# Kernel optimization log

Measured on AMD Instinct MI355X. Metric: run time of the kernel, lower is better.

Reference implementation:

```python
import jax, jax.numpy as jnp
import numpy as np
import math

B, NPG, DEG = 100, 500, 12          # graphs, nodes/graph, avg degree
F_IN, H, C = 128, 128, 10
RATIO = 0.5
N = B * NPG
E = N * DEG
K1 = math.ceil(NPG * RATIO)          # 250
K2 = math.ceil(K1 * RATIO)           # 125
K3 = math.ceil(K2 * RATIO)           # 63


def _lin(k, i, o):
    return jax.random.uniform(k, (i, o), jnp.float32, -1.0, 1.0) / np.sqrt(i).astype(np.float32)


def setup_inputs() -> dict:
    key = jax.random.key(0)
    ks = jax.random.split(key, 16)
    x = jax.random.normal(ks[0], (N, F_IN), jnp.float32)
    off = (jnp.arange(B, dtype=jnp.int32) * NPG)[:, None]
    src = (jax.random.randint(ks[1], (B, NPG * DEG), 0, NPG, jnp.int32) + off).reshape(-1)
    dst = (jax.random.randint(ks[2], (B, NPG * DEG), 0, NPG, jnp.int32) + off).reshape(-1)
    edge_index = jnp.stack([src, dst])
    return {
        'x': x, 'edge_index': edge_index,
        'Wl1': _lin(ks[3], F_IN, H), 'bl1': jnp.zeros((H,), jnp.float32), 'Wr1': _lin(ks[4], F_IN, H),
        'Wl2': _lin(ks[5], H, H), 'bl2': jnp.zeros((H,), jnp.float32), 'Wr2': _lin(ks[6], H, H),
        'Wl3': _lin(ks[7], H, H), 'bl3': jnp.zeros((H,), jnp.float32), 'Wr3': _lin(ks[8], H, H),
        'pw1': jax.random.normal(ks[9], (H,), jnp.float32),
        'pw2': jax.random.normal(ks[10], (H,), jnp.float32),
        'pw3': jax.random.normal(ks[11], (H,), jnp.float32),
        'W1': _lin(ks[12], 2 * H, H), 'b1': jnp.zeros((H,), jnp.float32),
        'W2': _lin(ks[13], H, H // 2), 'b2': jnp.zeros((H // 2,), jnp.float32),
        'W3': _lin(ks[14], H // 2, C), 'b3': jnp.zeros((C,), jnp.float32),
    }


def sage_conv(x, src, dst, emask, Wl, bl, Wr, n_nodes):
    # PyG SAGEConv: out_i = lin_l(mean_{j->i} x_j) + lin_r(x_i)
    msg = x[src] * emask[:, None]                                   # [E, d]
    agg = jax.ops.segment_sum(msg, dst, num_segments=n_nodes)
    cnt = jax.ops.segment_sum(emask, dst, num_segments=n_nodes)
    mean = agg / jnp.maximum(cnt, 1.0)[:, None]
    return mean @ Wl + bl + x @ Wr


def topk_pool(x, w, src, dst, emask, n_per, k):
    # TopKPooling: score = tanh(x.w/||w||); keep top-k nodes per graph; x_kept *= score
    score = jnp.tanh((x @ w) / jnp.linalg.norm(w))                  # [B*n_per]
    topv, topi = jax.lax.top_k(score.reshape(B, n_per), k)          # [B, k]
    perm = (topi + (jnp.arange(B, dtype=jnp.int32) * n_per)[:, None]).reshape(-1)
    x_new = x[perm] * topv.reshape(-1)[:, None]                     # [B*k, d]
    mapping = jnp.full((B * n_per,), -1, jnp.int32).at[perm].set(jnp.arange(B * k, dtype=jnp.int32))
    ns, nd = mapping[src], mapping[dst]
    emask_new = emask * ((ns >= 0) & (nd >= 0)).astype(emask.dtype)
    return x_new, jnp.maximum(ns, 0), jnp.maximum(nd, 0), emask_new


def readout(x, k):
    # global_max_pool || global_mean_pool (all graphs have exactly k nodes)
    xr = x.reshape(B, k, H)
    return jnp.concatenate([xr.max(axis=1), xr.mean(axis=1)], axis=1)  # [B, 2H]


def reference(x, edge_index, Wl1, bl1, Wr1, Wl2, bl2, Wr2, Wl3, bl3, Wr3,
              pw1, pw2, pw3, W1, b1, W2, b2, W3, b3):
    src, dst = edge_index[0], edge_index[1]
    emask = jnp.ones((E,), jnp.float32)
    h = jax.nn.relu(sage_conv(x, src, dst, emask, Wl1, bl1, Wr1, N))
    h, src, dst, emask = topk_pool(h, pw1, src, dst, emask, NPG, K1)
    x1 = readout(h, K1)
    h = jax.nn.relu(sage_conv(h, src, dst, emask, Wl2, bl2, Wr2, B * K1))
    h, src, dst, emask = topk_pool(h, pw2, src, dst, emask, K1, K2)
    x2 = readout(h, K2)
    h = jax.nn.relu(sage_conv(h, src, dst, emask, Wl3, bl3, Wr3, B * K2))
    h, src, dst, emask = topk_pool(h, pw3, src, dst, emask, K2, K3)
    x3 = readout(h, K3)
    z = x1 + x2 + x3
    z = jax.nn.relu(z @ W1 + b1)   # dropout is identity in eval mode
    z = jax.nn.relu(z @ W2 + b2)
    return jax.nn.log_softmax(z @ W3 + b3, axis=1)   # pool_loss == 0 for TopKPool
```

## Files before the change

kernel.cpp:

```cpp
#include <hip/hip_runtime.h>
#include <math.h>

#define BG    100
#define NPG   500
#define FD    128
#define EE    600000
#define EPG   6000
#define NN    50000
#define K1    250
#define K2    125
#define K3    63
#define CAP   64

typedef short v8s __attribute__((ext_vector_type(8)));
typedef float v4f __attribute__((ext_vector_type(4)));

__device__ __forceinline__ int swz(int p, int N) {
    int j = p & 7, i = p >> 3;
    int chunk = N >> 3, rem = N & 7;
    int mj = j < rem ? j : rem;
    return j * chunk + mj + i;
}

__device__ __forceinline__ unsigned short f2bf(float f) {
    unsigned int u = __float_as_uint(f);
    unsigned int r = (u + 0x7FFFu + ((u >> 16) & 1u)) >> 16;
    return (unsigned short)r;
}
__device__ __forceinline__ float bf2f(unsigned short b) {
    return __uint_as_float(((unsigned int)b) << 16);
}

__global__ __launch_bounds__(1024) void prep_fill_kernel(
        const int* __restrict__ ei, int* __restrict__ deg, int* __restrict__ col,
        const float* __restrict__ Wl1, const float* __restrict__ Wr1,
        const float* __restrict__ Wl2, const float* __restrict__ Wr2,
        const float* __restrict__ Wl3, const float* __restrict__ Wr3,
        unsigned short* __restrict__ wt_hi, unsigned short* __restrict__ wt_lo) {
    __shared__ int lcnt[NPG];
    int tid = threadIdx.x;
    if (blockIdx.x < BG) {
        int b = swz(blockIdx.x, BG);
        for (int i = tid; i < NPG; i += 1024) lcnt[i] = 0;
        __syncthreads();
        for (int e0 = tid; e0 < EPG; e0 += 1024) {
            int e = b * EPG + e0;
            int d = ei[EE + e];
            int pos = atomicAdd(&lcnt[d - b * NPG], 1);
            if (pos < CAP) col[(long long)d * CAP + pos] = ei[e];
        }
        __syncthreads();
        for (int i = tid; i < NPG; i += 1024) deg[b * NPG + i] = lcnt[i];
    } else {
        int id = (blockIdx.x - BG) * 1024 + tid;
        if (id >= 3 * 256 * 128) return;
        int layer = id >> 15, rem = id & 32767;
        int k = rem >> 7, n = rem & 127;
        const float* Wl = layer == 0 ? Wl1 : (layer == 1 ? Wl2 : Wl3);
        const float* Wr = layer == 0 ? Wr1 : (layer == 1 ? Wr2 : Wr3);
        float w = (k < 128) ? Wl[k * 128 + n] : Wr[(k - 128) * 128 + n];
        unsigned short hi = f2bf(w);
        unsigned short lo = f2bf(w - bf2f(hi));
        long long o = (long long)layer * 32768
                    + (long long)(k >> 5) * 4096
                    + (long long)(n >> 4) * 512
                    + (long long)((k >> 3) & 3) * 128
                    + (long long)(n & 15) * 8
                    + (k & 7);
        wt_hi[o] = hi;
        wt_lo[o] = lo;
    }
}

__global__ void gather_agg_kernel(const int* __restrict__ deg, const int* __restrict__ col,
                                  const float* __restrict__ x, float* __restrict__ mean,
                                  int n, int NB) {
    int g = swz(blockIdx.x, NB) * 256 + threadIdx.x;
    int node = g >> 5, sub = g & 31;
    if (node >= n) return;
    int d = deg[node]; if (d > CAP) d = CAP;
    const int* cp = col + (long long)node * CAP;
    float ax = 0.0f, ay = 0.0f, az = 0.0f, aw = 0.0f;
    int j = 0;
    for (; j + 8 <= d; j += 8) {
        float4 v0 = ((const float4*)(x + (long long)cp[j]     * FD))[sub];
        float4 v1 = ((const float4*)(x + (long long)cp[j + 1] * FD))[sub];
        float4 v2 = ((const float4*)(x + (long long)cp[j + 2] * FD))[sub];
        float4 v3 = ((const float4*)(x + (long long)cp[j + 3] * FD))[sub];
        float4 v4 = ((const float4*)(x + (long long)cp[j + 4] * FD))[sub];
        float4 v5 = ((const float4*)(x + (long long)cp[j + 5] * FD))[sub];
        float4 v6 = ((const float4*)(x + (long long)cp[j + 6] * FD))[sub];
        float4 v7 = ((const float4*)(x + (long long)cp[j + 7] * FD))[sub];
        ax += v0.x; ay += v0.y; az += v0.z; aw += v0.w;
        ax += v1.x; ay += v1.y; az += v1.z; aw += v1.w;
        ax += v2.x; ay += v2.y; az += v2.z; aw += v2.w;
        ax += v3.x; ay += v3.y; az += v3.z; aw += v3.w;
        ax += v4.x; ay += v4.y; az += v4.z; aw += v4.w;
        ax += v5.x; ay += v5.y; az += v5.z; aw += v5.w;
        ax += v6.x; ay += v6.y; az += v6.z; aw += v6.w;
        ax += v7.x; ay += v7.y; az += v7.z; aw += v7.w;
    }
    for (; j + 4 <= d; j += 4) {
        float4 v0 = ((const float4*)(x + (long long)cp[j]     * FD))[sub];
        float4 v1 = ((const float4*)(x + (long long)cp[j + 1] * FD))[sub];
        float4 v2 = ((const float4*)(x + (long long)cp[j + 2] * FD))[sub];
        float4 v3 = ((const float4*)(x + (long long)cp[j + 3] * FD))[sub];
        ax += v0.x; ay += v0.y; az += v0.z; aw += v0.w;
        ax += v1.x; ay += v1.y; az += v1.z; aw += v1.w;
        ax += v2.x; ay += v2.y; az += v2.z; aw += v2.w;
        ax += v3.x; ay += v3.y; az += v3.z; aw += v3.w;
    }
    for (; j < d; ++j) {
        float4 v = ((const float4*)(x + (long long)cp[j] * FD))[sub];
        ax += v.x; ay += v.y; az += v.z; aw += v.w;
    }
    float inv = 1.0f / fmaxf((float)d, 1.0f);
    float4 o; o.x = ax * inv; o.y = ay * inv; o.z = az * inv; o.w = aw * inv;
    ((float4*)(mean + (long long)node * FD))[sub] = o;
}

__global__ __launch_bounds__(512) void sage_gemm_mfma_kernel(
        const float* __restrict__ mean, const float* __restrict__ x,
        const unsigned short* __restrict__ wt_hi, const unsigned short* __restrict__ wt_lo,
        const float* __restrict__ bl, const float* __restrict__ pw,
        float* __restrict__ hout, float* __restrict__ score, int M, int NB) {
    __shared__ unsigned short Bh[4096], Bl[4096];
    __shared__ float spart[128 * 16];
    __shared__ float snrmp[16];
    int tid  = threadIdx.x;
    int wave = tid >> 6, lane = tid & 63;
    int quad = lane >> 4, l15 = lane & 15;
    int row0 = swz(blockIdx.x, NB) * 128;

    v4f acc[8];
#pragma unroll
    for (int t = 0; t < 8; t++) acc[t] = (v4f){0.f, 0.f, 0.f, 0.f};

    if (tid < 16) {
        float s = 0.f;
#pragma unroll
        for (int t = 0; t < 8; t++) { float p = pw[t * 16 + tid]; s += p * p; }
        snrmp[tid] = s;
    }

    int growA = row0 + 16 * wave + l15; if (growA > M - 1) growA = M - 1;

    for (int kt = 0; kt < 8; ++kt) {
        uint4 gh = ((const uint4*)(wt_hi + kt * 4096))[tid];
        uint4 gl = ((const uint4*)(wt_lo + kt * 4096))[tid];
        const float* Ab = (kt < 4) ? mean : x;
        const float* ap = Ab + (long long)growA * FD + ((kt < 4) ? kt : kt - 4) * 32 + quad * 8;
        float4 v0 = *(const float4*)(ap);
        float4 v1 = *(const float4*)(ap + 4);
        *(uint4*)&Bh[tid * 8] = gh;
        *(uint4*)&Bl[tid * 8] = gl;
        float f[8] = {v0.x, v0.y, v0.z, v0.w, v1.x, v1.y, v1.z, v1.w};
        v8s a_h, a_l;
#pragma unroll
        for (int q = 0; q < 8; q++) {
            unsigned short hb = f2bf(f[q]);
            a_h[q] = (short)hb;
            a_l[q] = (short)f2bf(f[q] - bf2f(hb));
        }
        __syncthreads();
#pragma unroll
        for (int t = 0; t < 8; t++) {
            v8s b_h = *(const v8s*)&Bh[t * 512 + lane * 8];
            v8s b_l = *(const v8s*)&Bl[t * 512 + lane * 8];
            acc[t] = __builtin_amdgcn_mfma_f32_16x16x32_bf16(a_l, b_h, acc[t], 0, 0, 0);
            acc[t] = __builtin_amdgcn_mfma_f32_16x16x32_bf16(a_h, b_l, acc[t], 0, 0, 0);
            acc[t] = __builtin_amdgcn_mfma_f32_16x16x32_bf16(a_h, b_h, acc[t], 0, 0, 0);
        }
        __syncthreads();
    }

    int rbase = row0 + 16 * wave + quad * 4;
    float part[4] = {0.f, 0.f, 0.f, 0.f};
#pragma unroll
    for (int t = 0; t < 8; t++) {
        int colc = t * 16 + l15;
        float blv = bl[colc];
        float pwv = pw[colc];
#pragma unroll
        for (int reg = 0; reg < 4; reg++) {
            float h = fmaxf(acc[t][reg] + blv, 0.0f);
            part[reg] += h * pwv;
            int grow = rbase + reg;
            if (grow < M) hout[(long long)grow * FD + colc] = h;
        }
    }
#pragma unroll
    for (int reg = 0; reg < 4; reg++)
        spart[(16 * wave + quad * 4 + reg) * 16 + l15] = part[reg];
    __syncthreads();
    if (tid < 128) {
        int grow = row0 + tid;
        if (grow < M) {
            float dot = 0.0f;
#pragma unroll
            for (int i = 0; i < 16; i++) dot += spart[tid * 16 + i];
            float nr = 0.0f;
#pragma unroll
            for (int i = 0; i < 16; i++) nr += snrmp[i];
            score[grow] = tanhf(dot / sqrtf(nr));
        }
    }
}

__global__ __launch_bounds__(1024) void topk_tail_kernel(
        const float* __restrict__ score, const float* __restrict__ hout,
        int n_per, int k, int SN,
        float* __restrict__ xp,
        const int* __restrict__ esrc, const int* __restrict__ edst,
        int* __restrict__ gmap,
        int* __restrict__ next_deg, int* __restrict__ next_col,
        float* __restrict__ z, int mode,
        const float* __restrict__ W1, const float* __restrict__ b1,
        const float* __restrict__ W2, const float* __restrict__ b2,
        const float* __restrict__ W3, const float* __restrict__ b3,
        float* __restrict__ out) {
    __shared__ float skey[512];
    __shared__ int   sidx[512];
    __shared__ unsigned long long spk[512];
    __shared__ int   lmap[512];
    __shared__ int   lcnt[512];
    __shared__ float pmax[1024];
    __shared__ float psum[1024];
    __shared__ float zs[256], t1[128], t2[64], t3[16];
    int tid = threadIdx.x;
    int kind, b;
    if (mode == 2) { kind = 1; b = swz(blockIdx.x, BG); }
    else {
        kind = blockIdx.x >= BG ? 1 : 0;
        b = swz(kind ? blockIdx.x - BG : blockIdx.x, BG);
    }

    if (kind == 0)
        for (int i = tid; i < SN; i += 1024) { lmap[i] = -1; lcnt[i] = 0; }

    unsigned long long P = 0ULL;
    if (tid < SN) {
        float keyv; unsigned int idx;
        if (tid < n_per) { keyv = score[b * n_per + tid]; idx = (unsigned int)tid; }
        else             { keyv = -INFINITY;              idx = 0x7fffffffu; }
        unsigned int u = __float_as_uint(keyv);
        u = (u & 0x80000000u) ? ~u : (u | 0x80000000u);
        P = ((unsigned long long)u << 32) | (unsigned long long)(~idx);
    }
    for (int ks = 2; ks <= SN; ks <<= 1) {
        for (int j = ks >> 1; j > 0; j >>= 1) {
            unsigned long long Q;
            if (j >= 64) {
                __syncthreads();
                if (tid < SN) spk[tid] = P;
                __syncthreads();
                Q = (tid < SN) ? spk[tid ^ j] : 0ULL;
            } else {
                Q = __shfl_xor(P, j, 64);
            }
            if (tid < SN) {
                bool keepmax = (((tid & ks) == 0) == ((tid & j) == 0));
                if (keepmax == (Q > P)) P = Q;
            }
        }
    }
    if (tid < SN) {
        unsigned int u  = (unsigned int)(P >> 32);
        unsigned int fb = (u & 0x80000000u) ? (u & 0x7fffffffu) : ~u;
        int iv = (int)(~(unsigned int)P);
        skey[tid] = __uint_as_float(fb);
        sidx[tid] = iv;
        if (kind == 0 && tid < k) lmap[iv] = tid;
    }
    __syncthreads();

    if (kind == 0) {
        int kbase = b * k;
        if (mode == 0) {
            int nbase = b * n_per;
            for (int e0 = tid; e0 < EPG; e0 += 1024) {
                int e = b * EPG + e0;
                int ls = lmap[esrc[e] - nbase];
                int ld = lmap[edst[e] - nbase];
                if (ls >= 0 && ld >= 0) {
                    int pos = atomicAdd(&lcnt[ld], 1);
                    if (pos < CAP) next_col[(long long)(kbase + ld) * CAP + pos] = kbase + ls;
                }
            }
            __syncthreads();
            for (int i = tid; i < NPG; i += 1024) {
                int l = lmap[i];
                gmap[nbase + i] = l >= 0 ? kbase + l : -1;
            }
        } else {
            int kb1 = b * n_per;
            for (int e0 = tid; e0 < EPG; e0 += 1024) {
                int e = b * EPG + e0;
                int ws = gmap[esrc[e]];
                int wd = gmap[edst[e]];
                int ls = (ws >= 0) ? lmap[ws - kb1] : -1;
                int ld = (wd >= 0) ? lmap[wd - kb1] : -1;
                if (ls >= 0 && ld >= 0) {
                    int pos = atomicAdd(&lcnt[ld], 1);
                    if (pos < CAP) next_col[(long long)(kbase + ld) * CAP + pos] = kbase + ls;
                }
            }
            __syncthreads();
        }
        for (int i = tid; i < k; i += 1024) next_deg[kbase + i] = lcnt[i];
        return;
    }

    int c = tid & 127, s = tid >> 7;
    float mx = -INFINITY, sm = 0.0f;
    {
        int r = s;
        long long hbase = (long long)b * n_per * FD + c;
        long long xbase = (long long)b * k * FD + c;
        for (; r + 24 < k; r += 32) {
            int i0 = sidx[r], i1 = sidx[r + 8], i2 = sidx[r + 16], i3 = sidx[r + 24];
            float k0 = skey[r], k1 = skey[r + 8], k2 = skey[r + 16], k3 = skey[r + 24];
            float v0 = hout[hbase + (long long)i0 * FD] * k0;
            float v1 = hout[hbase + (long long)i1 * FD] * k1;
            float v2 = hout[hbase + (long long)i2 * FD] * k2;
            float v3 = hout[hbase + (long long)i3 * FD] * k3;
            if (mode != 2) {
                xp[xbase + (long long)(r)      * FD] = v0;
                xp[xbase + (long long)(r + 8)  * FD] = v1;
                xp[xbase + (long long)(r + 16) * FD] = v2;
                xp[xbase + (long long)(r + 24) * FD] = v3;
            }
            mx = fmaxf(mx, v0); sm += v0;
            mx = fmaxf(mx, v1); sm += v1;
            mx = fmaxf(mx, v2); sm += v2;
            mx = fmaxf(mx, v3); sm += v3;
        }
        for (; r < k; r += 8) {
            float v = hout[hbase + (long long)sidx[r] * FD] * skey[r];
            if (mode != 2) xp[xbase + (long long)r * FD] = v;
            mx = fmaxf(mx, v); sm += v;
        }
    }
    pmax[tid] = mx; psum[tid] = sm;
    __syncthreads();
    if (tid < 128) {
        float m = -INFINITY, su = 0.0f;
#pragma unroll
        for (int i = 0; i < 8; i++) {
            m = fmaxf(m, pmax[i * 128 + tid]);
            su += psum[i * 128 + tid];
        }
        float mean = su / (float)k;
        if (mode == 0)      { z[b * 256 + tid] = m;  z[b * 256 + 128 + tid] = mean;  }
        else if (mode == 1) { z[b * 256 + tid] += m; z[b * 256 + 128 + tid] += mean; }
        else {
            zs[tid]       = z[b * 256 + tid] + m;
            zs[128 + tid] = z[b * 256 + 128 + tid] + mean;
        }
    }
    if (mode == 2) {
        __syncthreads();
        if (tid < 128) {
            float a = b1[tid];
            for (int kk = 0; kk < 256; kk++) a += zs[kk] * W1[kk * 128 + tid];
            t1[tid] = fmaxf(a, 0.0f);
        }
        __syncthreads();
        if (tid < 64) {
            float a = b2[tid];
            for (int kk = 0; kk < 128; kk++) a += t1[kk] * W2[kk * 64 + tid];
            t2[tid] = fmaxf(a, 0.0f);
        }
        __syncthreads();
        if (tid < 10) {
            float a = b3[tid];
            for (int kk = 0; kk < 64; kk++) a += t2[kk] * W3[kk * 10 + tid];
            t3[tid] = a;
        }
        __syncthreads();
        if (tid == 0) {
            float m = -INFINITY;
            for (int i = 0; i < 10; i++) m = fmaxf(m, t3[i]);
            float su = 0.0f;
            for (int i = 0; i < 10; i++) su += expf(t3[i] - m);
            float ls = logf(su);
            for (int i = 0; i < 10; i++) out[b * 10 + i] = t3[i] - m - ls;
        }
    }
}

extern "C" void kernel_launch(void* const* d_in, const int* in_sizes, int n_in,
                              void* d_out, int out_size, void* d_ws, size_t ws_size,
                              hipStream_t stream) {
    (void)in_sizes; (void)n_in; (void)out_size; (void)ws_size;
    const float* x   = (const float*)d_in[0];
    const int*   ei  = (const int*)d_in[1];
    const float* Wl1 = (const float*)d_in[2];
    const float* bl1 = (const float*)d_in[3];
    const float* Wr1 = (const float*)d_in[4];
    const float* Wl2 = (const float*)d_in[5];
    const float* bl2 = (const float*)d_in[6];
    const float* Wr2 = (const float*)d_in[7];
    const float* Wl3 = (const float*)d_in[8];
    const float* bl3 = (const float*)d_in[9];
    const float* Wr3 = (const float*)d_in[10];
    const float* pw1 = (const float*)d_in[11];
    const float* pw2 = (const float*)d_in[12];
    const float* pw3 = (const float*)d_in[13];
    const float* W1  = (const float*)d_in[14];
    const float* b1  = (const float*)d_in[15];
    const float* W2  = (const float*)d_in[16];
    const float* b2  = (const float*)d_in[17];
    const float* W3  = (const float*)d_in[18];
    const float* b3  = (const float*)d_in[19];
    float* out = (float*)d_out;

    char* ws = (char*)d_ws;
    size_t off = 0;
    auto alloc = [&](size_t bytes) {
        char* p = ws + off;
        off = (off + bytes + 255) & ~(size_t)255;
        return p;
    };
    float* mean  = (float*)alloc((size_t)NN * FD * 4);
    float* hout  = (float*)alloc((size_t)NN * FD * 4);
    float* xp    = (float*)alloc((size_t)BG * K1 * FD * 4);
    float* sc    = (float*)alloc((size_t)NN * 4);
    int*   gmap  = (int*)  alloc((size_t)NN * 4);
    int*   deg   = (int*)  alloc((size_t)NN * 4);
    int*   colb  = (int*)  alloc((size_t)NN * CAP * 4);
    float* z     = (float*)alloc((size_t)BG * 256 * 4);
    unsigned short* wt_hi = (unsigned short*)alloc((size_t)3 * 32768 * 2);
    unsigned short* wt_lo = (unsigned short*)alloc((size_t)3 * 32768 * 2);

    prep_fill_kernel<<<BG + 96, 1024, 0, stream>>>(ei, deg, colb,
                                                   Wl1, Wr1, Wl2, Wr2, Wl3, Wr3, wt_hi, wt_lo);

    {
        int nb = (NN * 32 + 255) / 256;
        gather_agg_kernel<<<nb, 256, 0, stream>>>(deg, colb, x, mean, NN, nb);
    }
    {
        int nb = (NN + 127) / 128;
        sage_gemm_mfma_kernel<<<nb, 512, 0, stream>>>(mean, x, wt_hi, wt_lo,
                                                      bl1, pw1, hout, sc, NN, nb);
    }
    topk_tail_kernel<<<2 * BG, 1024, 0, stream>>>(sc, hout, NPG, K1, 512, xp,
                                                  ei, ei + EE, gmap, deg, colb,
                                                  z, 0, W1, b1, W2, b2, W3, b3, out);

    const int N2 = BG * K1;
    {
        int nb = (N2 * 32 + 255) / 256;
        gather_agg_kernel<<<nb, 256, 0, stream>>>(deg, colb, xp, mean, N2, nb);
    }
    {
        int nb = (N2 + 127) / 128;
        sage_gemm_mfma_kernel<<<nb, 512, 0, stream>>>(mean, xp, wt_hi + 32768, wt_lo + 32768,
                                                      bl2, pw2, hout, sc, N2, nb);
    }
    topk_tail_kernel<<<2 * BG, 1024, 0, stream>>>(sc, hout, K1, K2, 256, xp,
                                                  ei, ei + EE, gmap, deg, colb,
                                                  z, 1, W1, b1, W2, b2, W3, b3, out);

    const int N3 = BG * K2;
    {
        int nb = (N3 * 32 + 255) / 256;
        gather_agg_kernel<<<nb, 256, 0, stream>>>(deg, colb, xp, mean, N3, nb);
    }
    {
        int nb = (N3 + 127) / 128;
        sage_gemm_mfma_kernel<<<nb, 512, 0, stream>>>(mean, xp, wt_hi + 65536, wt_lo + 65536,
                                                      bl3, pw3, hout, sc, N3, nb);
    }
    topk_tail_kernel<<<BG, 1024, 0, stream>>>(sc, hout, K2, K3, 128, (float*)0,
                                              (const int*)0, (const int*)0, (int*)0,
                                              (int*)0, (int*)0,
                                              z, 2, W1, b1, W2, b2, W3, b3, out);
}
```

Measured before the change: 250.7 us.

## Fuse neighbor mean aggregation into SAGE MFMA GEMM kernel

Removes the separate gather/aggregate kernel and computes each 128-row tile's neighbor mean inside the GEMM kernel. Rows are staged 16 at a time through a shared slab, and each wave keeps its mean fragment in registers for the first four K-tiles. This avoids writing and re-reading the full mean buffer in global memory and saves a launch per layer. In exchange, the gather now runs with fewer concurrent waves, has 16 block-wide barriers per tile, and adds 32 floats of register pressure per thread, which may reduce latency hiding on the random gathers.

After: 270.8 us. 1.08x slower.

```diff
diff --git a/kernel.cpp b/kernel.cpp
--- a/kernel.cpp
+++ b/kernel.cpp
@@ -72,59 +72,14 @@
     }
 }
 
-__global__ void gather_agg_kernel(const int* __restrict__ deg, const int* __restrict__ col,
-                                  const float* __restrict__ x, float* __restrict__ mean,
-                                  int n, int NB) {
-    int g = swz(blockIdx.x, NB) * 256 + threadIdx.x;
-    int node = g >> 5, sub = g & 31;
-    if (node >= n) return;
-    int d = deg[node]; if (d > CAP) d = CAP;
-    const int* cp = col + (long long)node * CAP;
-    float ax = 0.0f, ay = 0.0f, az = 0.0f, aw = 0.0f;
-    int j = 0;
-    for (; j + 8 <= d; j += 8) {
-        float4 v0 = ((const float4*)(x + (long long)cp[j]     * FD))[sub];
-        float4 v1 = ((const float4*)(x + (long long)cp[j + 1] * FD))[sub];
-        float4 v2 = ((const float4*)(x + (long long)cp[j + 2] * FD))[sub];
-        float4 v3 = ((const float4*)(x + (long long)cp[j + 3] * FD))[sub];
-        float4 v4 = ((const float4*)(x + (long long)cp[j + 4] * FD))[sub];
-        float4 v5 = ((const float4*)(x + (long long)cp[j + 5] * FD))[sub];
-        float4 v6 = ((const float4*)(x + (long long)cp[j + 6] * FD))[sub];
-        float4 v7 = ((const float4*)(x + (long long)cp[j + 7] * FD))[sub];
-        ax += v0.x; ay += v0.y; az += v0.z; aw += v0.w;
-        ax += v1.x; ay += v1.y; az += v1.z; aw += v1.w;
-        ax += v2.x; ay += v2.y; az += v2.z; aw += v2.w;
-        ax += v3.x; ay += v3.y; az += v3.z; aw += v3.w;
-        ax += v4.x; ay += v4.y; az += v4.z; aw += v4.w;
-        ax += v5.x; ay += v5.y; az += v5.z; aw += v5.w;
-        ax += v6.x; ay += v6.y; az += v6.z; aw += v6.w;
-        ax += v7.x; ay += v7.y; az += v7.z; aw += v7.w;
-    }
-    for (; j + 4 <= d; j += 4) {
-        float4 v0 = ((const float4*)(x + (long long)cp[j]     * FD))[sub];
-        float4 v1 = ((const float4*)(x + (long long)cp[j + 1] * FD))[sub];
-        float4 v2 = ((const float4*)(x + (long long)cp[j + 2] * FD))[sub];
-        float4 v3 = ((const float4*)(x + (long long)cp[j + 3] * FD))[sub];
-        ax += v0.x; ay += v0.y; az += v0.z; aw += v0.w;
-        ax += v1.x; ay += v1.y; az += v1.z; aw += v1.w;
-        ax += v2.x; ay += v2.y; az += v2.z; aw += v2.w;
-        ax += v3.x; ay += v3.y; az += v3.z; aw += v3.w;
-    }
-    for (; j < d; ++j) {
-        float4 v = ((const float4*)(x + (long long)cp[j] * FD))[sub];
-        ax += v.x; ay += v.y; az += v.z; aw += v.w;
-    }
-    float inv = 1.0f / fmaxf((float)d, 1.0f);
-    float4 o; o.x = ax * inv; o.y = ay * inv; o.z = az * inv; o.w = aw * inv;
-    ((float4*)(mean + (long long)node * FD))[sub] = o;
-}
-
-__global__ __launch_bounds__(512) void sage_gemm_mfma_kernel(
-        const float* __restrict__ mean, const float* __restrict__ x,
+__global__ __launch_bounds__(512) void sage_gemm_fused_kernel(
+        const int* __restrict__ deg, const int* __restrict__ col,
+        const float* __restrict__ x,
         const unsigned short* __restrict__ wt_hi, const unsigned short* __restrict__ wt_lo,
         const float* __restrict__ bl, const float* __restrict__ pw,
         float* __restrict__ hout, float* __restrict__ score, int M, int NB) {
     __shared__ unsigned short Bh[4096], Bl[4096];
+    __shared__ float mslab[16 * 132];
     __shared__ float spart[128 * 16];
     __shared__ float snrmp[16];
     int tid  = threadIdx.x;
@@ -145,11 +100,93 @@
 
     int growA = row0 + 16 * wave + l15; if (growA > M - 1) growA = M - 1;
 
-    for (int kt = 0; kt < 8; ++kt) {
+    float macc[32];
+    {
+        int rlocal = tid >> 5;
+        int sub    = tid & 31;
+        for (int rg = 0; rg < 8; ++rg) {
+            int row = row0 + rg * 16 + rlocal;
+            int d = (row < M) ? deg[row] : 0;
+            if (d > CAP) d = CAP;
+            const int* cp = col + (long long)row * CAP;
+            float ax = 0.0f, ay = 0.0f, az = 0.0f, aw = 0.0f;
+            int j = 0;
+            for (; j + 8 <= d; j += 8) {
+                float4 v0 = ((const float4*)(x + (long long)cp[j]     * FD))[sub];
+                float4 v1 = ((const float4*)(x + (long long)cp[j + 1] * FD))[sub];
+                float4 v2 = ((const float4*)(x + (long long)cp[j + 2] * FD))[sub];
+                float4 v3 = ((const float4*)(x + (long long)cp[j + 3] * FD))[sub];
+                float4 v4 = ((const float4*)(x + (long long)cp[j + 4] * FD))[sub];
+                float4 v5 = ((const float4*)(x + (long long)cp[j + 5] * FD))[sub];
+                float4 v6 = ((const float4*)(x + (long long)cp[j + 6] * FD))[sub];
+                float4 v7 = ((const float4*)(x + (long long)cp[j + 7] * FD))[sub];
+                ax += v0.x; ay += v0.y; az += v0.z; aw += v0.w;
+                ax += v1.x; ay += v1.y; az += v1.z; aw += v1.w;
+                ax += v2.x; ay += v2.y; az += v2.z; aw += v2.w;
+                ax += v3.x; ay += v3.y; az += v3.z; aw += v3.w;
+                ax += v4.x; ay += v4.y; az += v4.z; aw += v4.w;
+                ax += v5.x; ay += v5.y; az += v5.z; aw += v5.w;
+                ax += v6.x; ay += v6.y; az += v6.z; aw += v6.w;
+                ax += v7.x; ay += v7.y; az += v7.z; aw += v7.w;
+            }
+            for (; j + 4 <= d; j += 4) {
+                float4 v0 = ((const float4*)(x + (long long)cp[j]     * FD))[sub];
+                float4 v1 = ((const float4*)(x + (long long)cp[j + 1] * FD))[sub];
+                float4 v2 = ((const float4*)(x + (long long)cp[j + 2] * FD))[sub];
+                float4 v3 = ((const float4*)(x + (long long)cp[j + 3] * FD))[sub];
+                ax += v0.x; ay += v0.y; az += v0.z; aw += v0.w;
+                ax += v1.x; ay += v1.y; az += v1.z; aw += v1.w;
+                ax += v2.x; ay += v2.y; az += v2.z; aw += v2.w;
+                ax += v3.x; ay += v3.y; az += v3.z; aw += v3.w;
+            }
+            for (; j < d; ++j) {
+                float4 v = ((const float4*)(x + (long long)cp[j] * FD))[sub];
+                ax += v.x; ay += v.y; az += v.z; aw += v.w;
+            }
+            float inv = 1.0f / fmaxf((float)d, 1.0f);
+            float4 o; o.x = ax * inv; o.y = ay * inv; o.z = az * inv; o.w = aw * inv;
+            *(float4*)&mslab[rlocal * 132 + sub * 4] = o;
+            __syncthreads();
+            if (wave == rg) {
+#pragma unroll
+                for (int kt = 0; kt < 4; ++kt)
+#pragma unroll
+                    for (int q = 0; q < 8; ++q)
+                        macc[kt * 8 + q] = mslab[l15 * 132 + quad * 8 + kt * 32 + q];
+            }
+            __syncthreads();
+        }
+    }
+
+#pragma unroll
+    for (int kt = 0; kt < 4; ++kt) {
         uint4 gh = ((const uint4*)(wt_hi + kt * 4096))[tid];
         uint4 gl = ((const uint4*)(wt_lo + kt * 4096))[tid];
-        const float* Ab = (kt < 4) ? mean : x;
-        const float* ap = Ab + (long long)growA * FD + ((kt < 4) ? kt : kt - 4) * 32 + quad * 8;
+        *(uint4*)&Bh[tid * 8] = gh;
+        *(uint4*)&Bl[tid * 8] = gl;
+        v8s a_h, a_l;
+#pragma unroll
+        for (int q = 0; q < 8; q++) {
+            float fv = macc[kt * 8 + q];
+            unsigned short hb = f2bf(fv);
+            a_h[q] = (short)hb;
+            a_l[q] = (short)f2bf(fv - bf2f(hb));
+        }
+        __syncthreads();
+#pragma unroll
+        for (int t = 0; t < 8; t++) {
+            v8s b_h = *(const v8s*)&Bh[t * 512 + lane * 8];
+            v8s b_l = *(const v8s*)&Bl[t * 512 + lane * 8];
+            acc[t] = __builtin_amdgcn_mfma_f32_16x16x32_bf16(a_l, b_h, acc[t], 0, 0, 0);
+            acc[t] = __builtin_amdgcn_mfma_f32_16x16x32_bf16(a_h, b_l, acc[t], 0, 0, 0);
+            acc[t] = __builtin_amdgcn_mfma_f32_16x16x32_bf16(a_h, b_h, acc[t], 0, 0, 0);
+        }
+        __syncthreads();
+    }
+    for (int kt = 4; kt < 8; ++kt) {
+        uint4 gh = ((const uint4*)(wt_hi + kt * 4096))[tid];
+        uint4 gl = ((const uint4*)(wt_lo + kt * 4096))[tid];
+        const float* ap = x + (long long)growA * FD + (kt - 4) * 32 + quad * 8;
         float4 v0 = *(const float4*)(ap);
         float4 v1 = *(const float4*)(ap + 4);
         *(uint4*)&Bh[tid * 8] = gh;
@@ -422,7 +459,6 @@
         off = (off + bytes + 255) & ~(size_t)255;
         return p;
     };
-    float* mean  = (float*)alloc((size_t)NN * FD * 4);
     float* hout  = (float*)alloc((size_t)NN * FD * 4);
     float* xp    = (float*)alloc((size_t)BG * K1 * FD * 4);
     float* sc    = (float*)alloc((size_t)NN * 4);
@@ -437,13 +473,9 @@
                                                    Wl1, Wr1, Wl2, Wr2, Wl3, Wr3, wt_hi, wt_lo);
 
     {
-        int nb = (NN * 32 + 255) / 256;
-        gather_agg_kernel<<<nb, 256, 0, stream>>>(deg, colb, x, mean, NN, nb);
-    }
-    {
         int nb = (NN + 127) / 128;
-        sage_gemm_mfma_kernel<<<nb, 512, 0, stream>>>(mean, x, wt_hi, wt_lo,
-                                                      bl1, pw1, hout, sc, NN, nb);
+        sage_gemm_fused_kernel<<<nb, 512, 0, stream>>>(deg, colb, x, wt_hi, wt_lo,
+                                                       bl1, pw1, hout, sc, NN, nb);
     }
     topk_tail_kernel<<<2 * BG, 1024, 0, stream>>>(sc, hout, NPG, K1, 512, xp,
                                                   ei, ei + EE, gmap, deg, colb,
@@ -451,13 +483,9 @@
 
     const int N2 = BG * K1;
     {
-        int nb = (N2 * 32 + 255) / 256;
-        gather_agg_kernel<<<nb, 256, 0, stream>>>(deg, colb, xp, mean, N2, nb);
-    }
-    {
         int nb = (N2 + 127) / 128;
-        sage_gemm_mfma_kernel<<<nb, 512, 0, stream>>>(mean, xp, wt_hi + 32768, wt_lo + 32768,
-                                                      bl2, pw2, hout, sc, N2, nb);
+        sage_gemm_fused_kernel<<<nb, 512, 0, stream>>>(deg, colb, xp, wt_hi + 32768, wt_lo + 32768,
+                                                       bl2, pw2, hout, sc, N2, nb);
     }
     topk_tail_kernel<<<2 * BG, 1024, 0, stream>>>(sc, hout, K1, K2, 256, xp,
                                                   ei, ei + EE, gmap, deg, colb,
@@ -465,13 +493,9 @@
 
     const int N3 = BG * K2;
     {
-        int nb = (N3 * 32 + 255) / 256;
-        gather_agg_kernel<<<nb, 256, 0, stream>>>(deg, colb, xp, mean, N3, nb);
-    }
-    {
         int nb = (N3 + 127) / 128;
-        sage_gemm_mfma_kernel<<<nb, 512, 0, stream>>>(mean, xp, wt_hi + 65536, wt_lo + 65536,
-                                                      bl3, pw3, hout, sc, N3, nb);
+        sage_gemm_fused_kernel<<<nb, 512, 0, stream>>>(deg, colb, xp, wt_hi + 65536, wt_lo + 65536,
+                                                       bl3, pw3, hout, sc, N3, nb);
     }
     topk_tail_kernel<<<BG, 1024, 0, stream>>>(sc, hout, K2, K3, 128, (float*)0,
                                               (const int*)0, (const int*)0, (int*)0,
```

## Fuse pooling, layers 2-3 and MLP head into one per-graph kernel

Applied to the files above, without the earlier changes.

Replaces the three top-k tail kernels and the layer-2 and layer-3 gather and GEMM launches with a single kernel of one 1024-thread block per graph. Each block runs sort, edge remap, pooling, neighbour aggregation, the MFMA GEMM and the final MLP in sequence. The node remap stays in shared memory, and the next layer's scores stay on-chip instead of going through global memory. This removes several launches and global round trips. In exchange, the later layers run on only 100 blocks, so the gather and GEMM work gets less parallelism across the GPU.

After: 253.3 us. About the same (+1.0%).

```diff
diff --git a/kernel.cpp b/kernel.cpp
--- a/kernel.cpp
+++ b/kernel.cpp
@@ -207,42 +207,14 @@
     }
 }
 
-__global__ __launch_bounds__(1024) void topk_tail_kernel(
-        const float* __restrict__ score, const float* __restrict__ hout,
-        int n_per, int k, int SN,
-        float* __restrict__ xp,
-        const int* __restrict__ esrc, const int* __restrict__ edst,
-        int* __restrict__ gmap,
-        int* __restrict__ next_deg, int* __restrict__ next_col,
-        float* __restrict__ z, int mode,
-        const float* __restrict__ W1, const float* __restrict__ b1,
-        const float* __restrict__ W2, const float* __restrict__ b2,
-        const float* __restrict__ W3, const float* __restrict__ b3,
-        float* __restrict__ out) {
-    __shared__ float skey[512];
-    __shared__ int   sidx[512];
-    __shared__ unsigned long long spk[512];
-    __shared__ int   lmap[512];
-    __shared__ int   lcnt[512];
-    __shared__ float pmax[1024];
-    __shared__ float psum[1024];
-    __shared__ float zs[256], t1[128], t2[64], t3[16];
-    int tid = threadIdx.x;
-    int kind, b;
-    if (mode == 2) { kind = 1; b = swz(blockIdx.x, BG); }
-    else {
-        kind = blockIdx.x >= BG ? 1 : 0;
-        b = swz(kind ? blockIdx.x - BG : blockIdx.x, BG);
-    }
-
-    if (kind == 0)
-        for (int i = tid; i < SN; i += 1024) { lmap[i] = -1; lcnt[i] = 0; }
-
+
+__device__ __forceinline__ void sort_phase(const float* scoreSrc, int n_per, int SN, int tid,
+        unsigned long long* spk, float* skey, int* sidx, int* lmap, int kset) {
     unsigned long long P = 0ULL;
     if (tid < SN) {
         float keyv; unsigned int idx;
-        if (tid < n_per) { keyv = score[b * n_per + tid]; idx = (unsigned int)tid; }
-        else             { keyv = -INFINITY;              idx = 0x7fffffffu; }
+        if (tid < n_per) { keyv = scoreSrc[tid]; idx = (unsigned int)tid; }
+        else             { keyv = -INFINITY;     idx = 0x7fffffffu; }
         unsigned int u = __float_as_uint(keyv);
         u = (u & 0x80000000u) ? ~u : (u | 0x80000000u);
         P = ((unsigned long long)u << 32) | (unsigned long long)(~idx);
@@ -270,76 +242,38 @@
         int iv = (int)(~(unsigned int)P);
         skey[tid] = __uint_as_float(fb);
         sidx[tid] = iv;
-        if (kind == 0 && tid < k) lmap[iv] = tid;
-    }
-    __syncthreads();
-
-    if (kind == 0) {
-        int kbase = b * k;
-        if (mode == 0) {
-            int nbase = b * n_per;
-            for (int e0 = tid; e0 < EPG; e0 += 1024) {
-                int e = b * EPG + e0;
-                int ls = lmap[esrc[e] - nbase];
-                int ld = lmap[edst[e] - nbase];
-                if (ls >= 0 && ld >= 0) {
-                    int pos = atomicAdd(&lcnt[ld], 1);
-                    if (pos < CAP) next_col[(long long)(kbase + ld) * CAP + pos] = kbase + ls;
-                }
-            }
-            __syncthreads();
-            for (int i = tid; i < NPG; i += 1024) {
-                int l = lmap[i];
-                gmap[nbase + i] = l >= 0 ? kbase + l : -1;
-            }
-        } else {
-            int kb1 = b * n_per;
-            for (int e0 = tid; e0 < EPG; e0 += 1024) {
-                int e = b * EPG + e0;
-                int ws = gmap[esrc[e]];
-                int wd = gmap[edst[e]];
-                int ls = (ws >= 0) ? lmap[ws - kb1] : -1;
-                int ld = (wd >= 0) ? lmap[wd - kb1] : -1;
-                if (ls >= 0 && ld >= 0) {
-                    int pos = atomicAdd(&lcnt[ld], 1);
-                    if (pos < CAP) next_col[(long long)(kbase + ld) * CAP + pos] = kbase + ls;
-                }
-            }
-            __syncthreads();
-        }
-        for (int i = tid; i < k; i += 1024) next_deg[kbase + i] = lcnt[i];
-        return;
-    }
-
+        if (tid < kset) lmap[iv] = tid;
+    }
+}
+
+__device__ __forceinline__ void pool_phase(const float* __restrict__ hb, float* __restrict__ xb,
+        const float* skey, const int* sidx, float* pmax, float* psum,
+        float* zsum, float* zs, int k, int tid, int mode) {
     int c = tid & 127, s = tid >> 7;
     float mx = -INFINITY, sm = 0.0f;
-    {
-        int r = s;
-        long long hbase = (long long)b * n_per * FD + c;
-        long long xbase = (long long)b * k * FD + c;
-        for (; r + 24 < k; r += 32) {
-            int i0 = sidx[r], i1 = sidx[r + 8], i2 = sidx[r + 16], i3 = sidx[r + 24];
-            float k0 = skey[r], k1 = skey[r + 8], k2 = skey[r + 16], k3 = skey[r + 24];
-            float v0 = hout[hbase + (long long)i0 * FD] * k0;
-            float v1 = hout[hbase + (long long)i1 * FD] * k1;
-            float v2 = hout[hbase + (long long)i2 * FD] * k2;
-            float v3 = hout[hbase + (long long)i3 * FD] * k3;
-            if (mode != 2) {
-                xp[xbase + (long long)(r)      * FD] = v0;
-                xp[xbase + (long long)(r + 8)  * FD] = v1;
-                xp[xbase + (long long)(r + 16) * FD] = v2;
-                xp[xbase + (long long)(r + 24) * FD] = v3;
-            }
-            mx = fmaxf(mx, v0); sm += v0;
-            mx = fmaxf(mx, v1); sm += v1;
-            mx = fmaxf(mx, v2); sm += v2;
-            mx = fmaxf(mx, v3); sm += v3;
-        }
-        for (; r < k; r += 8) {
-            float v = hout[hbase + (long long)sidx[r] * FD] * skey[r];
-            if (mode != 2) xp[xbase + (long long)r * FD] = v;
-            mx = fmaxf(mx, v); sm += v;
-        }
+    int r = s;
+    for (; r + 24 < k; r += 32) {
+        int i0 = sidx[r], i1 = sidx[r + 8], i2 = sidx[r + 16], i3 = sidx[r + 24];
+        float k0 = skey[r], k1 = skey[r + 8], k2 = skey[r + 16], k3 = skey[r + 24];
+        float v0 = hb[c + (long long)i0 * FD] * k0;
+        float v1 = hb[c + (long long)i1 * FD] * k1;
+        float v2 = hb[c + (long long)i2 * FD] * k2;
+        float v3 = hb[c + (long long)i3 * FD] * k3;
+        if (xb) {
+            xb[c + (long long)(r)      * FD] = v0;
+            xb[c + (long long)(r + 8)  * FD] = v1;
+            xb[c + (long long)(r + 16) * FD] = v2;
+            xb[c + (long long)(r + 24) * FD] = v3;
+        }
+        mx = fmaxf(mx, v0); sm += v0;
+        mx = fmaxf(mx, v1); sm += v1;
+        mx = fmaxf(mx, v2); sm += v2;
+        mx = fmaxf(mx, v3); sm += v3;
+    }
+    for (; r < k; r += 8) {
+        float v = hb[c + (long long)sidx[r] * FD] * skey[r];
+        if (xb) xb[c + (long long)r * FD] = v;
+        mx = fmaxf(mx, v); sm += v;
     }
     pmax[tid] = mx; psum[tid] = sm;
     __syncthreads();
@@ -351,41 +285,276 @@
             su += psum[i * 128 + tid];
         }
         float mean = su / (float)k;
-        if (mode == 0)      { z[b * 256 + tid] = m;  z[b * 256 + 128 + tid] = mean;  }
-        else if (mode == 1) { z[b * 256 + tid] += m; z[b * 256 + 128 + tid] += mean; }
-        else {
-            zs[tid]       = z[b * 256 + tid] + m;
-            zs[128 + tid] = z[b * 256 + 128 + tid] + mean;
-        }
-    }
-    if (mode == 2) {
+        if (mode == 0)      { zsum[tid] = m;  zsum[128 + tid] = mean;  }
+        else if (mode == 1) { zsum[tid] += m; zsum[128 + tid] += mean; }
+        else { zs[tid] = zsum[tid] + m; zs[128 + tid] = zsum[128 + tid] + mean; }
+    }
+}
+
+__device__ __forceinline__ void gather_phase(const int* lcnt, const int* __restrict__ colX,
+        const float* __restrict__ xsrc, float* __restrict__ meanX,
+        int kbase, int k, int tid) {
+    int sub = tid & 31;
+    for (int base = 0; base < k; base += 32) {
+        int nl = base + (tid >> 5);
+        if (nl < k) {
+            int d = lcnt[nl]; if (d > CAP) d = CAP;
+            const int* cp = colX + (long long)(kbase + nl) * CAP;
+            float ax = 0.0f, ay = 0.0f, az = 0.0f, aw = 0.0f;
+            int j = 0;
+            for (; j + 8 <= d; j += 8) {
+                float4 v0 = ((const float4*)(xsrc + (long long)cp[j]     * FD))[sub];
+                float4 v1 = ((const float4*)(xsrc + (long long)cp[j + 1] * FD))[sub];
+                float4 v2 = ((const float4*)(xsrc + (long long)cp[j + 2] * FD))[sub];
+                float4 v3 = ((const float4*)(xsrc + (long long)cp[j + 3] * FD))[sub];
+                float4 v4 = ((const float4*)(xsrc + (long long)cp[j + 4] * FD))[sub];
+                float4 v5 = ((const float4*)(xsrc + (long long)cp[j + 5] * FD))[sub];
+                float4 v6 = ((const float4*)(xsrc + (long long)cp[j + 6] * FD))[sub];
+                float4 v7 = ((const float4*)(xsrc + (long long)cp[j + 7] * FD))[sub];
+                ax += v0.x; ay += v0.y; az += v0.z; aw += v0.w;
+                ax += v1.x; ay += v1.y; az += v1.z; aw += v1.w;
+                ax += v2.x; ay += v2.y; az += v2.z; aw += v2.w;
+                ax += v3.x; ay += v3.y; az += v3.z; aw += v3.w;
+                ax += v4.x; ay += v4.y; az += v4.z; aw += v4.w;
+                ax += v5.x; ay += v5.y; az += v5.z; aw += v5.w;
+                ax += v6.x; ay += v6.y; az += v6.z; aw += v6.w;
+                ax += v7.x; ay += v7.y; az += v7.z; aw += v7.w;
+            }
+            for (; j + 4 <= d; j += 4) {
+                float4 v0 = ((const float4*)(xsrc + (long long)cp[j]     * FD))[sub];
+                float4 v1 = ((const float4*)(xsrc + (long long)cp[j + 1] * FD))[sub];
+                float4 v2 = ((const float4*)(xsrc + (long long)cp[j + 2] * FD))[sub];
+                float4 v3 = ((const float4*)(xsrc + (long long)cp[j + 3] * FD))[sub];
+                ax += v0.x; ay += v0.y; az += v0.z; aw += v0.w;
+                ax += v1.x; ay += v1.y; az += v1.z; aw += v1.w;
+                ax += v2.x; ay += v2.y; az += v2.z; aw += v2.w;
+                ax += v3.x; ay += v3.y; az += v3.z; aw += v3.w;
+            }
+            for (; j < d; ++j) {
+                float4 v = ((const float4*)(xsrc + (long long)cp[j] * FD))[sub];
+                ax += v.x; ay += v.y; az += v.z; aw += v.w;
+            }
+            float inv = 1.0f / fmaxf((float)d, 1.0f);
+            float4 o; o.x = ax * inv; o.y = ay * inv; o.z = az * inv; o.w = aw * inv;
+            ((float4*)(meanX + (long long)(kbase + nl) * FD))[sub] = o;
+        }
+    }
+}
+
+__device__ __forceinline__ void gemm_phase(const float* __restrict__ meanX,
+        const float* __restrict__ xsrc,
+        const unsigned short* __restrict__ wh, const unsigned short* __restrict__ wl,
+        const float* __restrict__ blv, const float* __restrict__ pwv,
+        float* __restrict__ hX, float* scoreL, float* snrmp,
+        unsigned short* Bh, unsigned short* Bl, float* spart,
+        int kbase, int krows, int tid, int wave, int lane, int quad, int l15) {
+    v4f acc[8];
+#pragma unroll
+    for (int t = 0; t < 8; t++) acc[t] = (v4f){0.f, 0.f, 0.f, 0.f};
+    if (tid < 16) {
+        float s = 0.f;
+#pragma unroll
+        for (int t = 0; t < 8; t++) { float p = pwv[t * 16 + tid]; s += p * p; }
+        snrmp[tid] = s;
+    }
+    int rowEnd = kbase + krows;
+    int growA = kbase + 16 * wave + l15; if (growA > rowEnd - 1) growA = rowEnd - 1;
+    for (int kt = 0; kt < 8; ++kt) {
+        uint4 gh, gl;
+        if (tid < 512) {
+            gh = ((const uint4*)(wh + kt * 4096))[tid];
+            gl = ((const uint4*)(wl + kt * 4096))[tid];
+        }
+        const float* Ab = (kt < 4) ? meanX : xsrc;
+        const float* ap = Ab + (long long)growA * FD + ((kt < 4) ? kt : kt - 4) * 32 + quad * 8;
+        float4 v0 = *(const float4*)(ap);
+        float4 v1 = *(const float4*)(ap + 4);
+        if (tid < 512) {
+            *(uint4*)&Bh[tid * 8] = gh;
+            *(uint4*)&Bl[tid * 8] = gl;
+        }
+        float f[8] = {v0.x, v0.y, v0.z, v0.w, v1.x, v1.y, v1.z, v1.w};
+        v8s a_h, a_l;
+#pragma unroll
+        for (int q = 0; q < 8; q++) {
+            unsigned short hb2 = f2bf(f[q]);
+            a_h[q] = (short)hb2;
+            a_l[q] = (short)f2bf(f[q] - bf2f(hb2));
+        }
         __syncthreads();
-        if (tid < 128) {
-            float a = b1[tid];
-            for (int kk = 0; kk < 256; kk++) a += zs[kk] * W1[kk * 128 + tid];
-            t1[tid] = fmaxf(a, 0.0f);
+#pragma unroll
+        for (int t = 0; t < 8; t++) {
+            v8s b_h = *(const v8s*)&Bh[t * 512 + lane * 8];
+            v8s b_l = *(const v8s*)&Bl[t * 512 + lane * 8];
+            acc[t] = __builtin_amdgcn_mfma_f32_16x16x32_bf16(a_l, b_h, acc[t], 0, 0, 0);
+            acc[t] = __builtin_amdgcn_mfma_f32_16x16x32_bf16(a_h, b_l, acc[t], 0, 0, 0);
+            acc[t] = __builtin_amdgcn_mfma_f32_16x16x32_bf16(a_h, b_h, acc[t], 0, 0, 0);
         }
         __syncthreads();
-        if (tid < 64) {
-            float a = b2[tid];
-            for (int kk = 0; kk < 128; kk++) a += t1[kk] * W2[kk * 64 + tid];
-            t2[tid] = fmaxf(a, 0.0f);
+    }
+    int rbase = kbase + 16 * wave + quad * 4;
+    float part[4] = {0.f, 0.f, 0.f, 0.f};
+#pragma unroll
+    for (int t = 0; t < 8; t++) {
+        int colc = t * 16 + l15;
+        float blvv = blv[colc];
+        float pwvv = pwv[colc];
+#pragma unroll
+        for (int reg = 0; reg < 4; reg++) {
+            float h = fmaxf(acc[t][reg] + blvv, 0.0f);
+            part[reg] += h * pwvv;
+            int grow = rbase + reg;
+            if (grow < rowEnd) hX[(long long)grow * FD + colc] = h;
+        }
+    }
+#pragma unroll
+    for (int reg = 0; reg < 4; reg++)
+        spart[(16 * wave + quad * 4 + reg) * 16 + l15] = part[reg];
+    __syncthreads();
+    if (tid < krows) {
+        float dot = 0.0f;
+#pragma unroll
+        for (int i = 0; i < 16; i++) dot += spart[tid * 16 + i];
+        float nr = 0.0f;
+#pragma unroll
+        for (int i = 0; i < 16; i++) nr += snrmp[i];
+        scoreL[tid] = tanhf(dot / sqrtf(nr));
+    }
+}
+
+__global__ __launch_bounds__(1024) void mega_tail_kernel(
+        const float* __restrict__ sc1, const float* __restrict__ h1,
+        const int* __restrict__ ei,
+        float* __restrict__ xp2, float* __restrict__ xp3,
+        int* __restrict__ col2, int* __restrict__ col3,
+        float* __restrict__ mean2, float* __restrict__ mean3,
+        float* __restrict__ h2, float* __restrict__ h3,
+        const unsigned short* __restrict__ wt_hi, const unsigned short* __restrict__ wt_lo,
+        const float* __restrict__ bl2v, const float* __restrict__ pw2v,
+        const float* __restrict__ bl3v, const float* __restrict__ pw3v,
+        const float* __restrict__ W1, const float* __restrict__ b1,
+        const float* __restrict__ W2, const float* __restrict__ b2,
+        const float* __restrict__ W3, const float* __restrict__ b3,
+        float* __restrict__ out) {
+    __shared__ float skey[512];
+    __shared__ int   sidx[512];
+    __shared__ unsigned long long spk[512];
+    __shared__ int   lmap[512];
+    __shared__ int   lcnt[512];
+    __shared__ int   gmapL[NPG];
+    __shared__ float pmax[1024];
+    __shared__ float psum[1024];
+    __shared__ float zsum[256];
+    __shared__ float zs[256], t1[128], t2[64], t3[16];
+    __shared__ unsigned short Bh[4096], Bl[4096];
+    __shared__ float spart[256 * 16];
+    __shared__ float snrmp[16];
+    __shared__ float scoreL[256];
+
+    int tid = threadIdx.x;
+    int b = swz(blockIdx.x, BG);
+    int wave = tid >> 6, lane = tid & 63, quad = lane >> 4, l15 = lane & 15;
+    const int* esrc = ei;
+    const int* edst = ei + EE;
+    int nbase = b * NPG;
+
+    for (int i = tid; i < 512; i += 1024) { lmap[i] = -1; lcnt[i] = 0; }
+    __syncthreads();
+    sort_phase(sc1 + (long long)b * NPG, NPG, 512, tid, spk, skey, sidx, lmap, K1);
+    __syncthreads();
+    {
+        int kbase = b * K1;
+        for (int e0 = tid; e0 < EPG; e0 += 1024) {
+            int e = b * EPG + e0;
+            int ls = lmap[esrc[e] - nbase];
+            int ld = lmap[edst[e] - nbase];
+            if (ls >= 0 && ld >= 0) {
+                int pos = atomicAdd(&lcnt[ld], 1);
+                if (pos < CAP) col2[(long long)(kbase + ld) * CAP + pos] = kbase + ls;
+            }
         }
         __syncthreads();
-        if (tid < 10) {
-            float a = b3[tid];
-            for (int kk = 0; kk < 64; kk++) a += t2[kk] * W3[kk * 10 + tid];
-            t3[tid] = a;
-        }
-        __syncthreads();
-        if (tid == 0) {
-            float m = -INFINITY;
-            for (int i = 0; i < 10; i++) m = fmaxf(m, t3[i]);
-            float su = 0.0f;
-            for (int i = 0; i < 10; i++) su += expf(t3[i] - m);
-            float ls = logf(su);
-            for (int i = 0; i < 10; i++) out[b * 10 + i] = t3[i] - m - ls;
-        }
+        for (int i = tid; i < NPG; i += 1024) {
+            int l = lmap[i];
+            gmapL[i] = l >= 0 ? kbase + l : -1;
+        }
+    }
+    __syncthreads();
+    pool_phase(h1 + (long long)b * NPG * FD, xp2 + (long long)b * K1 * FD,
+               skey, sidx, pmax, psum, zsum, zs, K1, tid, 0);
+    __syncthreads();
+    __threadfence_block();
+
+    gather_phase(lcnt, col2, xp2, mean2, b * K1, K1, tid);
+    __syncthreads();
+    __threadfence_block();
+    gemm_phase(mean2, xp2, wt_hi + 32768, wt_lo + 32768, bl2v, pw2v,
+               h2, scoreL, snrmp, Bh, Bl, spart, b * K1, K1, tid, wave, lane, quad, l15);
+    __syncthreads();
+    __threadfence_block();
+
+    for (int i = tid; i < 256; i += 1024) { lmap[i] = -1; lcnt[i] = 0; }
+    __syncthreads();
+    sort_phase(scoreL, K1, 256, tid, spk, skey, sidx, lmap, K2);
+    __syncthreads();
+    {
+        int kbase = b * K2, kb1 = b * K1;
+        for (int e0 = tid; e0 < EPG; e0 += 1024) {
+            int e = b * EPG + e0;
+            int ws = gmapL[esrc[e] - nbase];
+            int wd = gmapL[edst[e] - nbase];
+            int ls = (ws >= 0) ? lmap[ws - kb1] : -1;
+            int ld = (wd >= 0) ? lmap[wd - kb1] : -1;
+            if (ls >= 0 && ld >= 0) {
+                int pos = atomicAdd(&lcnt[ld], 1);
+                if (pos < CAP) col3[(long long)(kbase + ld) * CAP + pos] = kbase + ls;
+            }
+        }
+    }
+    __syncthreads();
+    pool_phase(h2 + (long long)b * K1 * FD, xp3 + (long long)b * K2 * FD,
+               skey, sidx, pmax, psum, zsum, zs, K2, tid, 1);
+    __syncthreads();
+    __threadfence_block();
+
+    gather_phase(lcnt, col3, xp3, mean3, b * K2, K2, tid);
+    __syncthreads();
+    __threadfence_block();
+    gemm_phase(mean3, xp3, wt_hi + 65536, wt_lo + 65536, bl3v, pw3v,
+               h3, scoreL, snrmp, Bh, Bl, spart, b * K2, K2, tid, wave, lane, quad, l15);
+    __syncthreads();
+    __threadfence_block();
+
+    sort_phase(scoreL, K2, 128, tid, spk, skey, sidx, lmap, 0);
+    __syncthreads();
+    pool_phase(h3 + (long long)b * K2 * FD, (float*)0,
+               skey, sidx, pmax, psum, zsum, zs, K3, tid, 2);
+    __syncthreads();
+    if (tid < 128) {
+        float a = b1[tid];
+        for (int kk = 0; kk < 256; kk++) a += zs[kk] * W1[kk * 128 + tid];
+        t1[tid] = fmaxf(a, 0.0f);
+    }
+    __syncthreads();
+    if (tid < 64) {
+        float a = b2[tid];
+        for (int kk = 0; kk < 128; kk++) a += t1[kk] * W2[kk * 64 + tid];
+        t2[tid] = fmaxf(a, 0.0f);
+    }
+    __syncthreads();
+    if (tid < 10) {
+        float a = b3[tid];
+        for (int kk = 0; kk < 64; kk++) a += t2[kk] * W3[kk * 10 + tid];
+        t3[tid] = a;
+    }
+    __syncthreads();
+    if (tid == 0) {
+        float m = -INFINITY;
+        for (int i = 0; i < 10; i++) m = fmaxf(m, t3[i]);
+        float su = 0.0f;
+        for (int i = 0; i < 10; i++) su += expf(t3[i] - m);
+        float ls = logf(su);
+        for (int i = 0; i < 10; i++) out[b * 10 + i] = t3[i] - m - ls;
     }
 }
 
@@ -422,14 +591,21 @@
         off = (off + bytes + 255) & ~(size_t)255;
         return p;
     };
-    float* mean  = (float*)alloc((size_t)NN * FD * 4);
-    float* hout  = (float*)alloc((size_t)NN * FD * 4);
-    float* xp    = (float*)alloc((size_t)BG * K1 * FD * 4);
-    float* sc    = (float*)alloc((size_t)NN * 4);
-    int*   gmap  = (int*)  alloc((size_t)NN * 4);
+    const int N2 = BG * K1;
+    const int N3 = BG * K2;
+    float* mean1 = (float*)alloc((size_t)NN * FD * 4);
+    float* h1    = (float*)alloc((size_t)NN * FD * 4);
+    float* sc1   = (float*)alloc((size_t)NN * 4);
     int*   deg   = (int*)  alloc((size_t)NN * 4);
     int*   colb  = (int*)  alloc((size_t)NN * CAP * 4);
-    float* z     = (float*)alloc((size_t)BG * 256 * 4);
+    float* xp2   = (float*)alloc((size_t)N2 * FD * 4);
+    float* xp3   = (float*)alloc((size_t)N3 * FD * 4);
+    int*   col2  = (int*)  alloc((size_t)N2 * CAP * 4);
+    int*   col3  = (int*)  alloc((size_t)N3 * CAP * 4);
+    float* mean2 = (float*)alloc((size_t)N2 * FD * 4);
+    float* mean3 = (float*)alloc((size_t)N3 * FD * 4);
+    float* h2    = (float*)alloc((size_t)N2 * FD * 4);
+    float* h3    = (float*)alloc((size_t)N3 * FD * 4);
     unsigned short* wt_hi = (unsigned short*)alloc((size_t)3 * 32768 * 2);
     unsigned short* wt_lo = (unsigned short*)alloc((size_t)3 * 32768 * 2);
 
@@ -438,43 +614,16 @@
 
     {
         int nb = (NN * 32 + 255) / 256;
-        gather_agg_kernel<<<nb, 256, 0, stream>>>(deg, colb, x, mean, NN, nb);
+        gather_agg_kernel<<<nb, 256, 0, stream>>>(deg, colb, x, mean1, NN, nb);
     }
     {
         int nb = (NN + 127) / 128;
-        sage_gemm_mfma_kernel<<<nb, 512, 0, stream>>>(mean, x, wt_hi, wt_lo,
-                                                      bl1, pw1, hout, sc, NN, nb);
-    }
-    topk_tail_kernel<<<2 * BG, 1024, 0, stream>>>(sc, hout, NPG, K1, 512, xp,
-                                                  ei, ei + EE, gmap, deg, colb,
-                                                  z, 0, W1, b1, W2, b2, W3, b3, out);
-
-    const int N2 = BG * K1;
-    {
-        int nb = (N2 * 32 + 255) / 256;
-        gather_agg_kernel<<<nb, 256, 0, stream>>>(deg, colb, xp, mean, N2, nb);
-    }
-    {
-        int nb = (N2 + 127) / 128;
-        sage_gemm_mfma_kernel<<<nb, 512, 0, stream>>>(mean, xp, wt_hi + 32768, wt_lo + 32768,
-                                                      bl2, pw2, hout, sc, N2, nb);
-    }
-    topk_tail_kernel<<<2 * BG, 1024, 0, stream>>>(sc, hout, K1, K2, 256, xp,
-                                                  ei, ei + EE, gmap, deg, colb,
-                                                  z, 1, W1, b1, W2, b2, W3, b3, out);
-
-    const int N3 = BG * K2;
-    {
-        int nb = (N3 * 32 + 255) / 256;
-        gather_agg_kernel<<<nb, 256, 0, stream>>>(deg, colb, xp, mean, N3, nb);
-    }
-    {
-        int nb = (N3 + 127) / 128;
-        sage_gemm_mfma_kernel<<<nb, 512, 0, stream>>>(mean, xp, wt_hi + 65536, wt_lo + 65536,
-                                                      bl3, pw3, hout, sc, N3, nb);
-    }
-    topk_tail_kernel<<<BG, 1024, 0, stream>>>(sc, hout, K2, K3, 128, (float*)0,
-                                              (const int*)0, (const int*)0, (int*)0,
-                                              (int*)0, (int*)0,
-                                              z, 2, W1, b1, W2, b2, W3, b3, out);
-}
+        sage_gemm_mfma_kernel<<<nb, 512, 0, stream>>>(mean1, x, wt_hi, wt_lo,
+                                                      bl1, pw1, h1, sc1, NN, nb);
+    }
+
+    mega_tail_kernel<<<BG, 1024, 0, stream>>>(sc1, h1, ei,
+                                              xp2, xp3, col2, col3, mean2, mean3, h2, h3,
+                                              wt_hi, wt_lo, bl2, pw2, bl3, pw3,
+                                              W1, b1, W2, b2, W3, b3, out);
+}
```

## Double-buffer weight tiles and prefetch next K-slice in SAGE MFMA GEMM

Applied to the files above, without the earlier changes.

Makes the weight tiles in shared memory double-buffered and loads the next K-step's weights and activations into registers while the current step's MFMAs run. This drops one barrier per iteration and hides global load latency behind compute. It doubles shared-memory use for the B tiles, which may lower occupancy, and it raises register pressure.

Result: faster. 238.0 us (median of 2 runs) (-5.1%).

```diff
diff --git a/kernel.cpp b/kernel.cpp
--- a/kernel.cpp
+++ b/kernel.cpp
@@ -124,7 +124,7 @@
         const unsigned short* __restrict__ wt_hi, const unsigned short* __restrict__ wt_lo,
         const float* __restrict__ bl, const float* __restrict__ pw,
         float* __restrict__ hout, float* __restrict__ score, int M, int NB) {
-    __shared__ unsigned short Bh[4096], Bl[4096];
+    __shared__ unsigned short Bh[2][4096], Bl[2][4096];
     __shared__ float spart[128 * 16];
     __shared__ float snrmp[16];
     int tid  = threadIdx.x;
@@ -145,16 +145,17 @@
 
     int growA = row0 + 16 * wave + l15; if (growA > M - 1) growA = M - 1;
 
+    uint4 gh = ((const uint4*)(wt_hi))[tid];
+    uint4 gl = ((const uint4*)(wt_lo))[tid];
+    const float* ap0 = mean + (long long)growA * FD + quad * 8;
+    float4 av0 = *(const float4*)(ap0);
+    float4 av1 = *(const float4*)(ap0 + 4);
+    *(uint4*)&Bh[0][tid * 8] = gh;
+    *(uint4*)&Bl[0][tid * 8] = gl;
+
     for (int kt = 0; kt < 8; ++kt) {
-        uint4 gh = ((const uint4*)(wt_hi + kt * 4096))[tid];
-        uint4 gl = ((const uint4*)(wt_lo + kt * 4096))[tid];
-        const float* Ab = (kt < 4) ? mean : x;
-        const float* ap = Ab + (long long)growA * FD + ((kt < 4) ? kt : kt - 4) * 32 + quad * 8;
-        float4 v0 = *(const float4*)(ap);
-        float4 v1 = *(const float4*)(ap + 4);
-        *(uint4*)&Bh[tid * 8] = gh;
-        *(uint4*)&Bl[tid * 8] = gl;
-        float f[8] = {v0.x, v0.y, v0.z, v0.w, v1.x, v1.y, v1.z, v1.w};
+        int cur = kt & 1;
+        float f[8] = {av0.x, av0.y, av0.z, av0.w, av1.x, av1.y, av1.z, av1.w};
         v8s a_h, a_l;
 #pragma unroll
         for (int q = 0; q < 8; q++) {
@@ -162,16 +163,28 @@
             a_h[q] = (short)hb;
             a_l[q] = (short)f2bf(f[q] - bf2f(hb));
         }
+        if (kt < 7) {
+            gh = ((const uint4*)(wt_hi + (kt + 1) * 4096))[tid];
+            gl = ((const uint4*)(wt_lo + (kt + 1) * 4096))[tid];
+            const float* Ab = (kt + 1 < 4) ? mean : x;
+            const float* apn = Ab + (long long)growA * FD
+                             + ((kt + 1 < 4) ? (kt + 1) : (kt - 3)) * 32 + quad * 8;
+            av0 = *(const float4*)(apn);
+            av1 = *(const float4*)(apn + 4);
+        }
         __syncthreads();
 #pragma unroll
         for (int t = 0; t < 8; t++) {
-            v8s b_h = *(const v8s*)&Bh[t * 512 + lane * 8];
-            v8s b_l = *(const v8s*)&Bl[t * 512 + lane * 8];
+            v8s b_h = *(const v8s*)&Bh[cur][t * 512 + lane * 8];
+            v8s b_l = *(const v8s*)&Bl[cur][t * 512 + lane * 8];
             acc[t] = __builtin_amdgcn_mfma_f32_16x16x32_bf16(a_l, b_h, acc[t], 0, 0, 0);
             acc[t] = __builtin_amdgcn_mfma_f32_16x16x32_bf16(a_h, b_l, acc[t], 0, 0, 0);
             acc[t] = __builtin_amdgcn_mfma_f32_16x16x32_bf16(a_h, b_h, acc[t], 0, 0, 0);
         }
-        __syncthreads();
+        if (kt < 7) {
+            *(uint4*)&Bh[cur ^ 1][tid * 8] = gh;
+            *(uint4*)&Bl[cur ^ 1][tid * 8] = gl;
+        }
     }
 
     int rbase = row0 + 16 * wave + quad * 4;
```
